# Optimization experiments

Hardware: AMD Instinct MI355X
Metric: run time of the kernel (lower is better)

Reference implementation:

```python
import jax, jax.numpy as jnp
import numpy as np

B, C, L = 8, 512, 4096
KC, VC, H = 512, 512, 8
DK, DV = KC // H, VC // H
EPS = 1e-5


def _ln(x, g, b):
    m = jnp.mean(x, axis=-1, keepdims=True)
    v = jnp.var(x, axis=-1, keepdims=True)
    return (x - m) * jax.lax.rsqrt(v + EPS) * g + b


def setup_inputs() -> dict:
    key = jax.random.key(0)
    ks = jax.random.split(key, 12)
    s = 0.02
    return {
        "z1": jax.random.normal(ks[0], (B, C, L), jnp.float32),
        "z2": jax.random.normal(ks[1], (B, C, L), jnp.float32),
        "Wq": jax.random.normal(ks[2], (KC, C), jnp.float32) * s,
        "bq": jnp.zeros((KC,), jnp.float32),
        "Wk": jax.random.normal(ks[3], (KC, C), jnp.float32) * s,
        "bk": jnp.zeros((KC,), jnp.float32),
        "Wv": jax.random.normal(ks[4], (VC, C), jnp.float32) * s,
        "bv": jnp.zeros((VC,), jnp.float32),
        "Wr": jax.random.normal(ks[5], (C, VC), jnp.float32) * s,
        "br": jnp.zeros((C,), jnp.float32),
        "g1": jnp.ones((C,), jnp.float32),
        "be1": jnp.zeros((C,), jnp.float32),
        "W1": jax.random.normal(ks[6], (2 * C, C), jnp.float32) * s,
        "b1": jnp.zeros((2 * C,), jnp.float32),
        "W2": jax.random.normal(ks[7], (C, 2 * C), jnp.float32) * s,
        "b2": jnp.zeros((C,), jnp.float32),
        "g2": jnp.ones((C,), jnp.float32),
        "be2": jnp.zeros((C,), jnp.float32),
    }


def reference(z1, z2, Wq, bq, Wk, bk, Wv, bv, Wr, br, g1, be1, W1, b1, W2, b2, g2, be2):
    # 1x1 Conv1d projections (channels-first)
    q = jnp.einsum('oc,bcl->bol', Wq, z1) + bq[None, :, None]
    k = jnp.einsum('oc,bcl->bol', Wk, z2) + bk[None, :, None]
    v = jnp.einsum('oc,bcl->bol', Wv, z2) + bv[None, :, None]
    qh = q.reshape(B, H, DK, L)
    kh = k.reshape(B, H, DK, L)
    vh = v.reshape(B, H, DV, L)
    # efficient attention: keys softmax over length, queries over channels
    kh = jax.nn.softmax(kh, axis=-1)
    qh = jax.nn.softmax(qh, axis=2)
    ctx = jnp.einsum('bhkl,bhvl->bhkv', kh, vh)          # [B,H,DK,DV]
    att = jnp.einsum('bhkv,bhkl->bhvl', ctx, qh)          # [B,H,DV,L]
    att = att.reshape(B, VC, L)
    z = jnp.einsum('oc,bcl->bol', Wr, att) + br[None, :, None] + z1  # reprojection + residual
    # b c l -> b l c, LayerNorm, FFN, back
    x = z.transpose(0, 2, 1)
    x = _ln(x, g1, be1)
    h = jax.nn.elu(x @ W1.T + b1)
    y = h @ W2.T + b2
    y = _ln(y, g2, be2)
    return y.transpose(0, 2, 1)
```

## Files before the change

kernel.cpp:

```cpp
#include <hip/hip_runtime.h>
#include <math.h>

#define B_   8
#define C_   512
#define L_   4096
#define H_   8
#define DK_  64
#define C2_  1024

typedef unsigned short ushort;
typedef short     bf16x8_t __attribute__((ext_vector_type(8)));
typedef float     f32x4_t  __attribute__((ext_vector_type(4)));
typedef unsigned short u16x8 __attribute__((ext_vector_type(8)));
typedef unsigned short u16x4 __attribute__((ext_vector_type(4)));

__device__ __forceinline__ float bf2f(ushort u) {
    unsigned int x = ((unsigned int)u) << 16;
    float f; __builtin_memcpy(&f, &x, 4); return f;
}
__device__ __forceinline__ ushort f2bf(float f) {
    unsigned int x; __builtin_memcpy(&x, &f, 4);
    x = (x + 0x7FFFu + ((x >> 16) & 1u)) >> 16;
    return (ushort)x;
}

#define GLOAD_LDS16(gp, lp) \
    __builtin_amdgcn_global_load_lds((const __attribute__((address_space(1))) void*)(gp), \
                                     (__attribute__((address_space(3))) void*)(lp), 16, 0, 0)

__global__ __launch_bounds__(256) void transpose_in(const float* __restrict__ in,
                                                    ushort* __restrict__ out)
{
    const int b = blockIdx.z, c0 = blockIdx.y * 64, l0 = blockIdx.x * 64;
    __shared__ float t[64][65];
    const int tid = threadIdx.x;
    {
        const int c = tid >> 4, l4 = (tid & 15) * 4;
        const float* ip = in + ((size_t)b * C_ + c0) * L_ + l0;
#pragma unroll
        for (int cc = c; cc < 64; cc += 16) {
            float4 v = *(const float4*)(ip + (size_t)cc * L_ + l4);
            t[l4 + 0][cc] = v.x; t[l4 + 1][cc] = v.y;
            t[l4 + 2][cc] = v.z; t[l4 + 3][cc] = v.w;
        }
    }
    __syncthreads();
    {
        const int l = tid >> 3, c8 = (tid & 7) * 8;
        ushort* op = out + ((size_t)b * L_ + l0) * C_ + c0;
#pragma unroll
        for (int ll = l; ll < 64; ll += 32) {
            u16x8 v;
#pragma unroll
            for (int i = 0; i < 8; ++i) v[i] = f2bf(t[ll][c8 + i]);
            *(u16x8*)(op + (size_t)ll * C_ + c8) = v;
        }
    }
}

__global__ __launch_bounds__(256) void transpose_out(const float* __restrict__ in,
                                                     float* __restrict__ out)
{
    const int b = blockIdx.z, c0 = blockIdx.y * 64, l0 = blockIdx.x * 64;
    __shared__ float t[64][65];
    const int tid = threadIdx.x;
    {
        const int l = tid >> 4, c4 = (tid & 15) * 4;
#pragma unroll
        for (int ll = l; ll < 64; ll += 16) {
            float4 v = *(const float4*)(in + ((size_t)(b * L_ + l0 + ll)) * C_ + c0 + c4);
            t[c4 + 0][ll] = v.x; t[c4 + 1][ll] = v.y;
            t[c4 + 2][ll] = v.z; t[c4 + 3][ll] = v.w;
        }
    }
    __syncthreads();
    {
        const int c = tid >> 4, l4 = (tid & 15) * 4;
        float* op = out + ((size_t)b * C_ + c0) * L_ + l0;
#pragma unroll
        for (int cc = c; cc < 64; cc += 16) {
            float4 v = {t[cc][l4], t[cc][l4 + 1], t[cc][l4 + 2], t[cc][l4 + 3]};
            *(float4*)(op + (size_t)cc * L_ + l4) = v;
        }
    }
}

__global__ __launch_bounds__(256) void cvt_bf16(const float* __restrict__ in,
                                                ushort* __restrict__ out, int n4)
{
    const int i = blockIdx.x * 256 + threadIdx.x;
    if (i < n4) {
        float4 v = *(const float4*)(in + 4 * (size_t)i);
        u16x4 o; o[0] = f2bf(v.x); o[1] = f2bf(v.y); o[2] = f2bf(v.z); o[3] = f2bf(v.w);
        *(u16x4*)(out + 4 * (size_t)i) = o;
    }
}

__global__ __launch_bounds__(256) void zero_kernel(float* __restrict__ p, int n4)
{
    const int i = blockIdx.x * 256 + threadIdx.x;
    if (i < n4) { float4 z = {0.f, 0.f, 0.f, 0.f}; *(float4*)(p + 4 * (size_t)i) = z; }
}

template<int ACT, bool HAS_RES>
__global__ __launch_bounds__(256) void conv_mfma(
    const ushort* __restrict__ A, const ushort* __restrict__ Wt,
    const float* __restrict__ bias, const ushort* __restrict__ res,
    ushort* __restrict__ out, int M, int N, int K)
{
    const int m0 = blockIdx.x * 128;
    const int n0 = blockIdx.y * 128;
    const int tid = threadIdx.x;
    const int w = tid >> 6, lane = tid & 63;
    const int wm = (w & 1) * 64, wn = (w >> 1) * 64;
    const int l16 = lane & 15, quad = lane >> 4;

    __shared__ ushort smem[18432];

    f32x4_t acc[4][4];
#pragma unroll
    for (int i = 0; i < 4; ++i)
#pragma unroll
        for (int j = 0; j < 4; ++j) acc[i][j] = (f32x4_t){0.f, 0.f, 0.f, 0.f};

    const int srow = lane >> 2;
    const int sslot = lane & 3;

    const ushort* gA[2]; const ushort* gB[2];
    ushort* lA[2]; ushort* lB[2];
#pragma unroll
    for (int r = 0; r < 2; ++r) {
        const int row = r * 64 + w * 16 + srow;
        const int lk = sslot ^ ((row >> 2) & 3);
        gA[r] = A  + (size_t)(m0 + row) * K + lk * 8;
        gB[r] = Wt + (size_t)(n0 + row) * K + lk * 8;
        lA[r] = smem + (r * 64 + w * 16) * 32;
        lB[r] = smem + 4096 + (r * 64 + w * 16) * 32;
    }

    const int nt = K >> 5;

#pragma unroll
    for (int r = 0; r < 2; ++r) {
        GLOAD_LDS16(gA[r], lA[r]);
        GLOAD_LDS16(gB[r], lB[r]);
    }
    __syncthreads();

    for (int t = 0; t < nt; ++t) {
        const int cur = t & 1;
        if (t + 1 < nt) {
            const int nb = (cur ^ 1) * 8192;
            const size_t co = (size_t)(t + 1) * 32;
#pragma unroll
            for (int r = 0; r < 2; ++r) {
                GLOAD_LDS16(gA[r] + co, lA[r] + nb);
                GLOAD_LDS16(gB[r] + co, lB[r] + nb);
            }
        }
        const ushort* bA = smem + cur * 8192;
        const ushort* bB = bA + 4096;
        bf16x8_t amf[4], wf[4];
#pragma unroll
        for (int i = 0; i < 4; ++i) {
            const int arow = wm + i * 16 + l16;
            const int ap = quad ^ ((arow >> 2) & 3);
            amf[i] = *(const bf16x8_t*)(bA + arow * 32 + ap * 8);
            const int brow = wn + i * 16 + l16;
            const int bp = quad ^ ((brow >> 2) & 3);
            wf[i] = *(const bf16x8_t*)(bB + brow * 32 + bp * 8);
        }
#pragma unroll
        for (int i = 0; i < 4; ++i)
#pragma unroll
            for (int j = 0; j < 4; ++j)
                acc[i][j] = __builtin_amdgcn_mfma_f32_16x16x32_bf16(wf[j], amf[i], acc[i][j], 0, 0, 0);
        if (t + 1 < nt) __syncthreads();
    }

    __syncthreads();
    ushort* sT = smem + w * 4608;
#pragma unroll
    for (int j = 0; j < 4; ++j) {
        const int nb = wn + j * 16 + quad * 4;
        const float4 bo = *(const float4*)(bias + n0 + nb);
        const float bv[4] = {bo.x, bo.y, bo.z, bo.w};
#pragma unroll
        for (int i = 0; i < 4; ++i) {
            const int ml = i * 16 + l16;
            float v[4];
#pragma unroll
            for (int r = 0; r < 4; ++r) v[r] = acc[i][j][r] + bv[r];
            if (HAS_RES) {
                const u16x4 rv = *(const u16x4*)(res + (size_t)(m0 + wm + ml) * N + n0 + nb);
#pragma unroll
                for (int r = 0; r < 4; ++r) v[r] += bf2f(rv[r]);
            }
            if (ACT == 1) {
#pragma unroll
                for (int r = 0; r < 4; ++r) v[r] = (v[r] > 0.f) ? v[r] : (__expf(v[r]) - 1.f);
            }
            u16x4 pv;
#pragma unroll
            for (int r = 0; r < 4; ++r) pv[r] = f2bf(v[r]);
            *(u16x4*)(sT + ml * 72 + (nb - wn)) = pv;
        }
    }
    {
        const int rr = lane >> 3, ch = lane & 7;
#pragma unroll
        for (int rep = 0; rep < 8; ++rep) {
            const int ml = rep * 8 + rr;
            const u16x8 vo = *(const u16x8*)(sT + ml * 72 + ch * 8);
            *(u16x8*)(out + (size_t)(m0 + wm + ml) * N + n0 + wn + ch * 8) = vo;
        }
    }
}

__global__ __launch_bounds__(256) void kstat_chunk(const ushort* __restrict__ k,
                                                   float2* __restrict__ stats)
{
    const int cg = blockIdx.x;
    const int bc = blockIdx.y;
    const int b = bc >> 3, ch = bc & 7;
    const int tid = threadIdx.x;
    const int g = tid & 7;
    const int kk = tid >> 3;
    const int w = tid >> 6, lane = tid & 63;
    const ushort* base = k + ((size_t)(b * L_) + ch * 512) * C_ + cg * 64 + g * 8;

    __shared__ float red[4][8][8];
    __shared__ float mcol[64];

    float fm[8];
#pragma unroll
    for (int i = 0; i < 8; ++i) fm[i] = -3.0e38f;
    for (int r = kk; r < 512; r += 32) {
        u16x8 v = *(const u16x8*)(base + (size_t)r * C_);
#pragma unroll
        for (int i = 0; i < 8; ++i) fm[i] = fmaxf(fm[i], bf2f(v[i]));
    }
#pragma unroll
    for (int off = 8; off <= 32; off <<= 1)
#pragma unroll
        for (int i = 0; i < 8; ++i) fm[i] = fmaxf(fm[i], __shfl_xor(fm[i], off));
    if ((lane >> 3) == 0)
#pragma unroll
        for (int i = 0; i < 8; ++i) red[w][g][i] = fm[i];
    __syncthreads();
    if (tid < 64) {
        const int g2 = tid >> 3, j = tid & 7;
        mcol[g2 * 8 + j] = fmaxf(fmaxf(red[0][g2][j], red[1][g2][j]),
                                 fmaxf(red[2][g2][j], red[3][g2][j]));
    }
    __syncthreads();
    float fmc[8];
#pragma unroll
    for (int i = 0; i < 8; ++i) fmc[i] = mcol[g * 8 + i];

    float fs[8] = {};
    for (int r = kk; r < 512; r += 32) {
        u16x8 v = *(const u16x8*)(base + (size_t)r * C_);
#pragma unroll
        for (int i = 0; i < 8; ++i) fs[i] += __expf(bf2f(v[i]) - fmc[i]);
    }
#pragma unroll
    for (int off = 8; off <= 32; off <<= 1)
#pragma unroll
        for (int i = 0; i < 8; ++i) fs[i] += __shfl_xor(fs[i], off);
    __syncthreads();
    if ((lane >> 3) == 0)
#pragma unroll
        for (int i = 0; i < 8; ++i) red[w][g][i] = fs[i];
    __syncthreads();
    if (tid < 64) {
        const int g2 = tid >> 3, j = tid & 7;
        const float s = red[0][g2][j] + red[1][g2][j] + red[2][g2][j] + red[3][g2][j];
        const int c = cg * 64 + g2 * 8 + j;
        stats[((size_t)(b * C_ + c)) * 8 + ch] = make_float2(mcol[g2 * 8 + j], s);
    }
}

__global__ __launch_bounds__(256) void kstat_merge(const float2* __restrict__ stats,
                                                   float2* __restrict__ minv)
{
    const int i = blockIdx.x * 256 + threadIdx.x;
    if (i >= B_ * C_) return;
    float2 st[8];
    float m = -3.0e38f;
#pragma unroll
    for (int ch = 0; ch < 8; ++ch) { st[ch] = stats[(size_t)i * 8 + ch]; m = fmaxf(m, st[ch].x); }
    float s = 0.f;
#pragma unroll
    for (int ch = 0; ch < 8; ++ch) s += st[ch].y * __expf(st[ch].x - m);
    minv[i] = make_float2(m, 1.f / s);
}

__global__ __launch_bounds__(256) void ctx_accum(
    const ushort* __restrict__ kk, const ushort* __restrict__ vv,
    const float2* __restrict__ minv, float* __restrict__ ctx)
{
    const int bh = blockIdx.y, b = bh >> 3, h = bh & 7;
    const int l0 = blockIdx.x * 512;
    const int tid = threadIdx.x;
    __shared__ float sK[32][72];
    __shared__ float sV[32][72];
    const int srow = tid >> 3, c8 = (tid & 7) * 8;
    const int dv4 = (tid & 15) * 4, dk4 = (tid >> 4) * 4;

    float2 cst[8];
    {
        const float2* mp = minv + (size_t)b * C_ + h * 64 + c8;
#pragma unroll
        for (int i = 0; i < 8; ++i) cst[i] = mp[i];
    }
    float acc[4][4] = {};

    for (int lt = 0; lt < 512; lt += 32) {
        const size_t gbase = ((size_t)(b * L_ + l0 + lt + srow)) * C_ + h * 64 + c8;
        u16x8 kv = *(const u16x8*)(kk + gbase);
        u16x8 vvv = *(const u16x8*)(vv + gbase);
        __syncthreads();
#pragma unroll
        for (int i = 0; i < 8; ++i) {
            sK[srow][c8 + i] = __expf(bf2f(kv[i]) - cst[i].x) * cst[i].y;
            sV[srow][c8 + i] = bf2f(vvv[i]);
        }
        __syncthreads();
#pragma unroll
        for (int ll = 0; ll < 32; ++ll) {
            const float4 a = *(const float4*)&sV[ll][dv4];
            const float4 bb = *(const float4*)&sK[ll][dk4];
            const float av[4] = {a.x, a.y, a.z, a.w};
            const float bv[4] = {bb.x, bb.y, bb.z, bb.w};
#pragma unroll
            for (int i = 0; i < 4; ++i)
#pragma unroll
                for (int j = 0; j < 4; ++j)
                    acc[i][j] = fmaf(av[i], bv[j], acc[i][j]);
        }
    }
    float* cp = ctx + (size_t)bh * 4096;
#pragma unroll
    for (int i = 0; i < 4; ++i)
#pragma unroll
        for (int j = 0; j < 4; ++j)
            atomicAdd(&cp[(dv4 + i) * 64 + (dk4 + j)], acc[i][j]);
}

__global__ __launch_bounds__(256) void att_mfma(
    const ushort* __restrict__ q, const float* __restrict__ ctx,
    ushort* __restrict__ att)
{
    const int bh = blockIdx.y, b = bh >> 3, h = bh & 7;
    const int l0 = blockIdx.x * 128;
    const int tid = threadIdx.x, w = tid >> 6, lane = tid & 63;
    const int l16 = lane & 15, quad = lane >> 4;

    __shared__ ushort sQ[128 * 72];
    __shared__ ushort sC[64 * 72];

    {
        const int part = tid & 7;
#pragma unroll
        for (int rr = tid >> 3; rr < 128; rr += 32) {
            u16x8 v = *(const u16x8*)(q + ((size_t)(b * L_ + l0 + rr)) * C_ + h * 64 + part * 8);
            float f[8], m = -3.0e38f;
#pragma unroll
            for (int i = 0; i < 8; ++i) { f[i] = bf2f(v[i]); m = fmaxf(m, f[i]); }
            m = fmaxf(m, __shfl_xor(m, 1));
            m = fmaxf(m, __shfl_xor(m, 2));
            m = fmaxf(m, __shfl_xor(m, 4));
            float s = 0.f;
#pragma unroll
            for (int i = 0; i < 8; ++i) { f[i] = __expf(f[i] - m); s += f[i]; }
            s += __shfl_xor(s, 1); s += __shfl_xor(s, 2); s += __shfl_xor(s, 4);
            const float inv = 1.f / s;
            u16x8 o;
#pragma unroll
            for (int i = 0; i < 8; ++i) o[i] = f2bf(f[i] * inv);
            *(u16x8*)(sQ + rr * 72 + part * 8) = o;
        }
        const int dv = tid >> 2, dk0 = (tid & 3) * 16;
        const float* cp = ctx + (size_t)bh * 4096 + dv * 64 + dk0;
#pragma unroll
        for (int i = 0; i < 16; ++i) sC[dv * 72 + dk0 + i] = f2bf(cp[i]);
    }
    __syncthreads();

    f32x4_t acc[2][4];
#pragma unroll
    for (int i = 0; i < 2; ++i)
#pragma unroll
        for (int j = 0; j < 4; ++j) acc[i][j] = (f32x4_t){0.f, 0.f, 0.f, 0.f};

#pragma unroll
    for (int ks = 0; ks < 2; ++ks) {
        const int k0 = ks * 32;
        bf16x8_t aq[2], bc[4];
#pragma unroll
        for (int i = 0; i < 2; ++i)
            aq[i] = *(const bf16x8_t*)(sQ + (w * 32 + i * 16 + l16) * 72 + k0 + quad * 8);
#pragma unroll
        for (int j = 0; j < 4; ++j)
            bc[j] = *(const bf16x8_t*)(sC + (j * 16 + l16) * 72 + k0 + quad * 8);
#pragma unroll
        for (int i = 0; i < 2; ++i)
#pragma unroll
            for (int j = 0; j < 4; ++j)
                acc[i][j] = __builtin_amdgcn_mfma_f32_16x16x32_bf16(aq[i], bc[j], acc[i][j], 0, 0, 0);
    }

#pragma unroll
    for (int j = 0; j < 4; ++j)
#pragma unroll
        for (int i = 0; i < 2; ++i) {
            const int mb = l0 + w * 32 + i * 16 + quad * 4;
#pragma unroll
            for (int r = 0; r < 4; ++r)
                att[((size_t)(b * L_ + mb + r)) * C_ + h * 64 + j * 16 + l16] = f2bf(acc[i][j][r]);
        }
}

template<bool OUTF32>
__global__ __launch_bounds__(256) void ln_row(
    const ushort* __restrict__ in, const float* __restrict__ g,
    const float* __restrict__ be, ushort* __restrict__ outb,
    float* __restrict__ outf)
{
    const int tid = threadIdx.x, w = tid >> 6, lane = tid & 63;
    const size_t row = (size_t)blockIdx.x * 4 + w;
    const ushort* p = in + row * C_ + lane * 8;
    u16x8 v = *(const u16x8*)p;
    float f[8], s = 0.f, s2 = 0.f;
#pragma unroll
    for (int i = 0; i < 8; ++i) { f[i] = bf2f(v[i]); s += f[i]; s2 = fmaf(f[i], f[i], s2); }
#pragma unroll
    for (int o = 1; o < 64; o <<= 1) { s += __shfl_xor(s, o); s2 += __shfl_xor(s2, o); }
    const float mean = s * (1.f / C_);
    const float var  = s2 * (1.f / C_) - mean * mean;
    const float inv  = rsqrtf(var + 1e-5f);
    if (OUTF32) {
        float* op = outf + row * C_ + lane * 8;
#pragma unroll
        for (int i = 0; i < 8; ++i)
            op[i] = (f[i] - mean) * inv * g[lane * 8 + i] + be[lane * 8 + i];
    } else {
        u16x8 ov;
#pragma unroll
        for (int i = 0; i < 8; ++i)
            ov[i] = f2bf((f[i] - mean) * inv * g[lane * 8 + i] + be[lane * 8 + i]);
        *(u16x8*)(outb + row * C_ + lane * 8) = ov;
    }
}

extern "C" void kernel_launch(void* const* d_in, const int* in_sizes, int n_in,
                              void* d_out, int out_size, void* d_ws, size_t ws_size,
                              hipStream_t stream)
{
    const float* z1  = (const float*)d_in[0];
    const float* z2  = (const float*)d_in[1];
    const float* Wq  = (const float*)d_in[2];
    const float* bq  = (const float*)d_in[3];
    const float* Wk  = (const float*)d_in[4];
    const float* bk  = (const float*)d_in[5];
    const float* Wv  = (const float*)d_in[6];
    const float* bv  = (const float*)d_in[7];
    const float* Wr  = (const float*)d_in[8];
    const float* br  = (const float*)d_in[9];
    const float* g1  = (const float*)d_in[10];
    const float* be1 = (const float*)d_in[11];
    const float* W1  = (const float*)d_in[12];
    const float* b1  = (const float*)d_in[13];
    const float* W2  = (const float*)d_in[14];
    const float* b2  = (const float*)d_in[15];
    const float* g2  = (const float*)d_in[16];
    const float* be2 = (const float*)d_in[17];
    float* out = (float*)d_out;

    const size_t SB = (size_t)B_ * L_ * C_;
    ushort* ws16 = (ushort*)d_ws;
    ushort* b0v = ws16;
    ushort* b1v = ws16 + SB;
    ushort* b2v = ws16 + 2 * SB;
    ushort* b3v = ws16 + 3 * SB;
    ushort* wb  = ws16 + 4 * SB;
    ushort* wbq = wb;
    ushort* wbk = wb + 262144;
    ushort* wbv = wb + 524288;
    ushort* wbr = wb + 786432;
    ushort* wb1 = wb + 1048576;
    ushort* wb2 = wb + 1572864;
    float*  ctxf = (float*)(wb + 2097152);
    float2* stats = (float2*)(ctxf + 65536);
    float2* minv  = stats + (size_t)B_ * C_ * 8;
    ushort* vbuf = (ushort*)d_out;
    ushort* hbuf = (ushort*)d_out;
    float*  yf32 = (float*)b2v;

    const dim3 blk(256);
    const int M = B_ * L_;

    transpose_in<<<dim3(L_/64, C_/64, B_), blk, 0, stream>>>(z1, b0v);
    transpose_in<<<dim3(L_/64, C_/64, B_), blk, 0, stream>>>(z2, b1v);
    cvt_bf16<<<dim3(262144/4/256), blk, 0, stream>>>(Wq, wbq, 262144/4);
    cvt_bf16<<<dim3(262144/4/256), blk, 0, stream>>>(Wk, wbk, 262144/4);
    cvt_bf16<<<dim3(262144/4/256), blk, 0, stream>>>(Wv, wbv, 262144/4);
    cvt_bf16<<<dim3(262144/4/256), blk, 0, stream>>>(Wr, wbr, 262144/4);
    cvt_bf16<<<dim3(524288/4/256), blk, 0, stream>>>(W1, wb1, 524288/4);
    cvt_bf16<<<dim3(524288/4/256), blk, 0, stream>>>(W2, wb2, 524288/4);

    conv_mfma<0,false><<<dim3(M/128, C_/128), blk, 0, stream>>>(b0v, wbq, bq, nullptr, b2v, M, C_, C_);
    conv_mfma<0,false><<<dim3(M/128, C_/128), blk, 0, stream>>>(b1v, wbk, bk, nullptr, b3v, M, C_, C_);
    conv_mfma<0,false><<<dim3(M/128, C_/128), blk, 0, stream>>>(b1v, wbv, bv, nullptr, vbuf, M, C_, C_);

    kstat_chunk<<<dim3(C_/64, B_ * 8), blk, 0, stream>>>(b3v, stats);
    kstat_merge<<<dim3((B_ * C_ + 255) / 256), blk, 0, stream>>>(stats, minv);

    zero_kernel<<<dim3(65536/256), blk, 0, stream>>>(ctxf, 65536);
    ctx_accum<<<dim3(8, B_ * H_), blk, 0, stream>>>(b3v, vbuf, minv, ctxf);

    att_mfma<<<dim3(L_/128, B_ * H_), blk, 0, stream>>>(b2v, ctxf, b1v);

    conv_mfma<0,true><<<dim3(M/128, C_/128), blk, 0, stream>>>(b1v, wbr, br, b0v, b2v, M, C_, C_);

    ln_row<false><<<dim3(M/4), blk, 0, stream>>>(b2v, g1, be1, b3v, nullptr);

    conv_mfma<1,false><<<dim3(M/128, C2_/128), blk, 0, stream>>>(b3v, wb1, b1, nullptr, hbuf, M, C2_, C_);

    conv_mfma<0,false><<<dim3(M/128, C_/128), blk, 0, stream>>>(hbuf, wb2, b2, nullptr, b0v, M, C_, C2_);

    ln_row<true><<<dim3(M/4), blk, 0, stream>>>(b0v, g2, be2, nullptr, yf32);

    transpose_out<<<dim3(L_/64, C_/64, B_), blk, 0, stream>>>(yf32, out);
}
```

Measured before the change: 577.7 us.

## Triple-buffer GEMM LDS loads with one barrier per step; split ctx_accum finer

```diff
diff --git a/kernel.cpp b/kernel.cpp
--- a/kernel.cpp
+++ b/kernel.cpp
@@ -115,7 +115,7 @@
     const int wm = (w & 1) * 64, wn = (w >> 1) * 64;
     const int l16 = lane & 15, quad = lane >> 4;
 
-    __shared__ ushort smem[18432];
+    __shared__ ushort smem[24576];
 
     f32x4_t acc[4][4];
 #pragma unroll
@@ -127,55 +127,62 @@
     const int sslot = lane & 3;
 
     const ushort* gA[2]; const ushort* gB[2];
-    ushort* lA[2]; ushort* lB[2];
+    int loff[2];
 #pragma unroll
     for (int r = 0; r < 2; ++r) {
         const int row = r * 64 + w * 16 + srow;
         const int lk = sslot ^ ((row >> 2) & 3);
         gA[r] = A  + (size_t)(m0 + row) * K + lk * 8;
         gB[r] = Wt + (size_t)(n0 + row) * K + lk * 8;
-        lA[r] = smem + (r * 64 + w * 16) * 32;
-        lB[r] = smem + 4096 + (r * 64 + w * 16) * 32;
+        loff[r] = (r * 64 + w * 16) * 32;
     }
 
     const int nt = K >> 5;
 
 #pragma unroll
-    for (int r = 0; r < 2; ++r) {
-        GLOAD_LDS16(gA[r], lA[r]);
-        GLOAD_LDS16(gB[r], lB[r]);
-    }
-    __syncthreads();
-
+    for (int p = 0; p < 2; ++p) {
+        ushort* lb = smem + p * 8192;
+#pragma unroll
+        for (int r = 0; r < 2; ++r) {
+            GLOAD_LDS16(gA[r] + p * 32, lb + loff[r]);
+            GLOAD_LDS16(gB[r] + p * 32, lb + 4096 + loff[r]);
+        }
+    }
+
+    int buf = 0;
     for (int t = 0; t < nt; ++t) {
-        const int cur = t & 1;
-        if (t + 1 < nt) {
-            const int nb = (cur ^ 1) * 8192;
-            const size_t co = (size_t)(t + 1) * 32;
+        if (t + 1 < nt) { asm volatile("s_waitcnt vmcnt(4)" ::: "memory"); }
+        else            { asm volatile("s_waitcnt vmcnt(0)" ::: "memory"); }
+        __builtin_amdgcn_s_barrier();
+        __builtin_amdgcn_sched_barrier(0);
+        if (t + 2 < nt) {
+            const int nb2 = (buf >= 1) ? buf - 1 : buf + 2;
+            ushort* lb = smem + nb2 * 8192;
+            const size_t co = (size_t)(t + 2) * 32;
 #pragma unroll
             for (int r = 0; r < 2; ++r) {
-                GLOAD_LDS16(gA[r] + co, lA[r] + nb);
-                GLOAD_LDS16(gB[r] + co, lB[r] + nb);
+                GLOAD_LDS16(gA[r] + co, lb + loff[r]);
+                GLOAD_LDS16(gB[r] + co, lb + 4096 + loff[r]);
             }
         }
-        const ushort* bA = smem + cur * 8192;
+        const ushort* bA = smem + buf * 8192;
         const ushort* bB = bA + 4096;
         bf16x8_t amf[4], wf[4];
 #pragma unroll
         for (int i = 0; i < 4; ++i) {
             const int arow = wm + i * 16 + l16;
-            const int ap = quad ^ ((arow >> 2) & 3);
-            amf[i] = *(const bf16x8_t*)(bA + arow * 32 + ap * 8);
+            amf[i] = *(const bf16x8_t*)(bA + arow * 32 + (quad ^ ((arow >> 2) & 3)) * 8);
             const int brow = wn + i * 16 + l16;
-            const int bp = quad ^ ((brow >> 2) & 3);
-            wf[i] = *(const bf16x8_t*)(bB + brow * 32 + bp * 8);
-        }
+            wf[i]  = *(const bf16x8_t*)(bB + brow * 32 + (quad ^ ((brow >> 2) & 3)) * 8);
+        }
+        __builtin_amdgcn_s_setprio(1);
 #pragma unroll
         for (int i = 0; i < 4; ++i)
 #pragma unroll
             for (int j = 0; j < 4; ++j)
                 acc[i][j] = __builtin_amdgcn_mfma_f32_16x16x32_bf16(wf[j], amf[i], acc[i][j], 0, 0, 0);
-        if (t + 1 < nt) __syncthreads();
+        __builtin_amdgcn_s_setprio(0);
+        buf = (buf == 2) ? 0 : buf + 1;
     }
 
     __syncthreads();
@@ -301,10 +308,10 @@
     const float2* __restrict__ minv, float* __restrict__ ctx)
 {
     const int bh = blockIdx.y, b = bh >> 3, h = bh & 7;
-    const int l0 = blockIdx.x * 512;
+    const int l0 = blockIdx.x * 256;
     const int tid = threadIdx.x;
-    __shared__ float sK[32][72];
-    __shared__ float sV[32][72];
+    __shared__ float sK[32][76];
+    __shared__ float sV[32][76];
     const int srow = tid >> 3, c8 = (tid & 7) * 8;
     const int dv4 = (tid & 15) * 4, dk4 = (tid >> 4) * 4;
 
@@ -316,16 +323,21 @@
     }
     float acc[4][4] = {};
 
-    for (int lt = 0; lt < 512; lt += 32) {
+    for (int lt = 0; lt < 256; lt += 32) {
         const size_t gbase = ((size_t)(b * L_ + l0 + lt + srow)) * C_ + h * 64 + c8;
         u16x8 kv = *(const u16x8*)(kk + gbase);
         u16x8 vvv = *(const u16x8*)(vv + gbase);
         __syncthreads();
+        float fk[8], fv[8];
 #pragma unroll
         for (int i = 0; i < 8; ++i) {
-            sK[srow][c8 + i] = __expf(bf2f(kv[i]) - cst[i].x) * cst[i].y;
-            sV[srow][c8 + i] = bf2f(vvv[i]);
-        }
+            fk[i] = __expf(bf2f(kv[i]) - cst[i].x) * cst[i].y;
+            fv[i] = bf2f(vvv[i]);
+        }
+        *(float4*)&sK[srow][c8]     = (float4){fk[0], fk[1], fk[2], fk[3]};
+        *(float4*)&sK[srow][c8 + 4] = (float4){fk[4], fk[5], fk[6], fk[7]};
+        *(float4*)&sV[srow][c8]     = (float4){fv[0], fv[1], fv[2], fv[3]};
+        *(float4*)&sV[srow][c8 + 4] = (float4){fv[4], fv[5], fv[6], fv[7]};
         __syncthreads();
 #pragma unroll
         for (int ll = 0; ll < 32; ++ll) {
@@ -518,7 +530,7 @@
     kstat_merge<<<dim3((B_ * C_ + 255) / 256), blk, 0, stream>>>(stats, minv);
 
     zero_kernel<<<dim3(65536/256), blk, 0, stream>>>(ctxf, 65536);
-    ctx_accum<<<dim3(8, B_ * H_), blk, 0, stream>>>(b3v, vbuf, minv, ctxf);
+    ctx_accum<<<dim3(16, B_ * H_), blk, 0, stream>>>(b3v, vbuf, minv, ctxf);
 
     att_mfma<<<dim3(L_/128, B_ * H_), blk, 0, stream>>>(b2v, ctxf, b1v);
 
```

After: 579.1 us. Within noise of the previous version (+0.2%).

## Enlarge GEMM tiles to 256x256 with 512 threads and move ctx accumulation to MFMA

Applied to the files above, without the earlier changes.

```diff
diff --git a/kernel.cpp b/kernel.cpp
--- a/kernel.cpp
+++ b/kernel.cpp
@@ -103,96 +103,97 @@
 }
 
 template<int ACT, bool HAS_RES>
-__global__ __launch_bounds__(256) void conv_mfma(
+__global__ __launch_bounds__(512, 2) void conv_mfma(
     const ushort* __restrict__ A, const ushort* __restrict__ Wt,
     const float* __restrict__ bias, const ushort* __restrict__ res,
     ushort* __restrict__ out, int M, int N, int K)
 {
-    const int m0 = blockIdx.x * 128;
-    const int n0 = blockIdx.y * 128;
+    const int m0 = blockIdx.x * 256;
+    const int n0 = blockIdx.y * 256;
     const int tid = threadIdx.x;
     const int w = tid >> 6, lane = tid & 63;
-    const int wm = (w & 1) * 64, wn = (w >> 1) * 64;
+    const int wm = (w >> 2) * 128, wn = (w & 3) * 64;
     const int l16 = lane & 15, quad = lane >> 4;
 
-    __shared__ ushort smem[18432];
-
-    f32x4_t acc[4][4];
-#pragma unroll
-    for (int i = 0; i < 4; ++i)
+    __shared__ ushort smem[32768];
+
+    const int sRow = tid >> 2;
+    const int sSwz = ((tid & 3) ^ (sRow & 3)) * 8;
+    const ushort* gA0 = A  + (size_t)(m0 + sRow) * K + sSwz;
+    const ushort* gA1 = A  + (size_t)(m0 + 128 + sRow) * K + sSwz;
+    const ushort* gB0 = Wt + (size_t)(n0 + sRow) * K + sSwz;
+    const ushort* gB1 = Wt + (size_t)(n0 + 128 + sRow) * K + sSwz;
+    const int dA0 = (w * 16) * 32;
+    const int dA1 = (128 + w * 16) * 32;
+
+    f32x4_t acc[8][4];
+#pragma unroll
+    for (int i = 0; i < 8; ++i)
 #pragma unroll
         for (int j = 0; j < 4; ++j) acc[i][j] = (f32x4_t){0.f, 0.f, 0.f, 0.f};
 
-    const int srow = lane >> 2;
-    const int sslot = lane & 3;
-
-    const ushort* gA[2]; const ushort* gB[2];
-    ushort* lA[2]; ushort* lB[2];
-#pragma unroll
-    for (int r = 0; r < 2; ++r) {
-        const int row = r * 64 + w * 16 + srow;
-        const int lk = sslot ^ ((row >> 2) & 3);
-        gA[r] = A  + (size_t)(m0 + row) * K + lk * 8;
-        gB[r] = Wt + (size_t)(n0 + row) * K + lk * 8;
-        lA[r] = smem + (r * 64 + w * 16) * 32;
-        lB[r] = smem + 4096 + (r * 64 + w * 16) * 32;
-    }
-
     const int nt = K >> 5;
 
-#pragma unroll
-    for (int r = 0; r < 2; ++r) {
-        GLOAD_LDS16(gA[r], lA[r]);
-        GLOAD_LDS16(gB[r], lB[r]);
-    }
-    __syncthreads();
+    {
+        ushort* bufA = smem;
+        ushort* bufB = smem + 8192;
+        GLOAD_LDS16(gA0, bufA + dA0);
+        GLOAD_LDS16(gA1, bufA + dA1);
+        GLOAD_LDS16(gB0, bufB + dA0);
+        GLOAD_LDS16(gB1, bufB + dA1);
+    }
 
     for (int t = 0; t < nt; ++t) {
-        const int cur = t & 1;
+        const ushort* bufA = smem + (t & 1) * 16384;
+        const ushort* bufB = bufA + 8192;
+        __builtin_amdgcn_s_barrier();
+        asm volatile("" ::: "memory");
         if (t + 1 < nt) {
-            const int nb = (cur ^ 1) * 8192;
+            ushort* nA = smem + ((t + 1) & 1) * 16384;
+            ushort* nB = nA + 8192;
             const size_t co = (size_t)(t + 1) * 32;
-#pragma unroll
-            for (int r = 0; r < 2; ++r) {
-                GLOAD_LDS16(gA[r] + co, lA[r] + nb);
-                GLOAD_LDS16(gB[r] + co, lB[r] + nb);
-            }
-        }
-        const ushort* bA = smem + cur * 8192;
-        const ushort* bB = bA + 4096;
-        bf16x8_t amf[4], wf[4];
-#pragma unroll
-        for (int i = 0; i < 4; ++i) {
-            const int arow = wm + i * 16 + l16;
-            const int ap = quad ^ ((arow >> 2) & 3);
-            amf[i] = *(const bf16x8_t*)(bA + arow * 32 + ap * 8);
-            const int brow = wn + i * 16 + l16;
-            const int bp = quad ^ ((brow >> 2) & 3);
-            wf[i] = *(const bf16x8_t*)(bB + brow * 32 + bp * 8);
-        }
-#pragma unroll
-        for (int i = 0; i < 4; ++i)
+            GLOAD_LDS16(gA0 + co, nA + dA0);
+            GLOAD_LDS16(gA1 + co, nA + dA1);
+            GLOAD_LDS16(gB0 + co, nB + dA0);
+            GLOAD_LDS16(gB1 + co, nB + dA1);
+            asm volatile("s_waitcnt vmcnt(4)" ::: "memory");
+        } else {
+            asm volatile("s_waitcnt vmcnt(0)" ::: "memory");
+        }
+        __builtin_amdgcn_s_barrier();
+        asm volatile("" ::: "memory");
+
+        bf16x8_t wf[4];
+#pragma unroll
+        for (int j = 0; j < 4; ++j) {
+            const int br = wn + j * 16 + l16;
+            wf[j] = *(const bf16x8_t*)(bufB + br * 32 + (quad ^ (br & 3)) * 8);
+        }
+        __builtin_amdgcn_s_setprio(1);
+#pragma unroll
+        for (int i = 0; i < 8; ++i) {
+            const int ar = wm + i * 16 + l16;
+            const bf16x8_t af = *(const bf16x8_t*)(bufA + ar * 32 + (quad ^ (ar & 3)) * 8);
 #pragma unroll
             for (int j = 0; j < 4; ++j)
-                acc[i][j] = __builtin_amdgcn_mfma_f32_16x16x32_bf16(wf[j], amf[i], acc[i][j], 0, 0, 0);
-        if (t + 1 < nt) __syncthreads();
-    }
-
-    __syncthreads();
-    ushort* sT = smem + w * 4608;
+                acc[i][j] = __builtin_amdgcn_mfma_f32_16x16x32_bf16(wf[j], af, acc[i][j], 0, 0, 0);
+        }
+        __builtin_amdgcn_s_setprio(0);
+    }
+
 #pragma unroll
     for (int j = 0; j < 4; ++j) {
-        const int nb = wn + j * 16 + quad * 4;
-        const float4 bo = *(const float4*)(bias + n0 + nb);
+        const int nb = n0 + wn + j * 16 + quad * 4;
+        const float4 bo = *(const float4*)(bias + nb);
         const float bv[4] = {bo.x, bo.y, bo.z, bo.w};
 #pragma unroll
-        for (int i = 0; i < 4; ++i) {
-            const int ml = i * 16 + l16;
+        for (int i = 0; i < 8; ++i) {
+            const int m = m0 + wm + i * 16 + l16;
             float v[4];
 #pragma unroll
             for (int r = 0; r < 4; ++r) v[r] = acc[i][j][r] + bv[r];
             if (HAS_RES) {
-                const u16x4 rv = *(const u16x4*)(res + (size_t)(m0 + wm + ml) * N + n0 + nb);
+                const u16x4 rv = *(const u16x4*)(res + (size_t)m * N + nb);
 #pragma unroll
                 for (int r = 0; r < 4; ++r) v[r] += bf2f(rv[r]);
             }
@@ -203,16 +204,7 @@
             u16x4 pv;
 #pragma unroll
             for (int r = 0; r < 4; ++r) pv[r] = f2bf(v[r]);
-            *(u16x4*)(sT + ml * 72 + (nb - wn)) = pv;
-        }
-    }
-    {
-        const int rr = lane >> 3, ch = lane & 7;
-#pragma unroll
-        for (int rep = 0; rep < 8; ++rep) {
-            const int ml = rep * 8 + rr;
-            const u16x8 vo = *(const u16x8*)(sT + ml * 72 + ch * 8);
-            *(u16x8*)(out + (size_t)(m0 + wm + ml) * N + n0 + wn + ch * 8) = vo;
+            *(u16x4*)(out + (size_t)m * N + nb) = pv;
         }
     }
 }
@@ -296,56 +288,76 @@
     minv[i] = make_float2(m, 1.f / s);
 }
 
-__global__ __launch_bounds__(256) void ctx_accum(
+__global__ __launch_bounds__(256) void ctx_mfma(
     const ushort* __restrict__ kk, const ushort* __restrict__ vv,
     const float2* __restrict__ minv, float* __restrict__ ctx)
 {
     const int bh = blockIdx.y, b = bh >> 3, h = bh & 7;
-    const int l0 = blockIdx.x * 512;
-    const int tid = threadIdx.x;
-    __shared__ float sK[32][72];
-    __shared__ float sV[32][72];
-    const int srow = tid >> 3, c8 = (tid & 7) * 8;
-    const int dv4 = (tid & 15) * 4, dk4 = (tid >> 4) * 4;
+    const int l0 = blockIdx.x * 256;
+    const int tid = threadIdx.x, w = tid >> 6, lane = tid & 63;
+    const int l16 = lane & 15, quad = lane >> 4;
+
+    __shared__ ushort sK[64 * 72];
+    __shared__ ushort sV[64 * 72];
+
+    const int grp = tid >> 7;
+    const int st  = tid & 127;
+    const int sc8 = (st & 7) * 8;
+    const int sl4 = (st >> 3) * 4;
+    const ushort* gsrc = (grp ? vv : kk)
+        + ((size_t)(b * L_ + l0 + sl4)) * C_ + h * 64 + sc8;
+    ushort* dst = grp ? sV : sK;
 
     float2 cst[8];
-    {
-        const float2* mp = minv + (size_t)b * C_ + h * 64 + c8;
-#pragma unroll
-        for (int i = 0; i < 8; ++i) cst[i] = mp[i];
-    }
-    float acc[4][4] = {};
-
-    for (int lt = 0; lt < 512; lt += 32) {
-        const size_t gbase = ((size_t)(b * L_ + l0 + lt + srow)) * C_ + h * 64 + c8;
-        u16x8 kv = *(const u16x8*)(kk + gbase);
-        u16x8 vvv = *(const u16x8*)(vv + gbase);
+#pragma unroll
+    for (int i = 0; i < 8; ++i)
+        cst[i] = minv[(size_t)b * C_ + h * 64 + sc8 + i];
+
+    f32x4_t acc[4];
+#pragma unroll
+    for (int j = 0; j < 4; ++j) acc[j] = (f32x4_t){0.f, 0.f, 0.f, 0.f};
+
+    for (int tile = 0; tile < 4; ++tile) {
+        u16x8 vr[4];
+#pragma unroll
+        for (int j = 0; j < 4; ++j)
+            vr[j] = *(const u16x8*)(gsrc + ((size_t)(tile * 64 + j)) * C_);
         __syncthreads();
-#pragma unroll
-        for (int i = 0; i < 8; ++i) {
-            sK[srow][c8 + i] = __expf(bf2f(kv[i]) - cst[i].x) * cst[i].y;
-            sV[srow][c8 + i] = bf2f(vvv[i]);
+        if (grp == 0) {
+#pragma unroll
+            for (int c = 0; c < 8; ++c) {
+                u16x4 o;
+#pragma unroll
+                for (int j = 0; j < 4; ++j)
+                    o[j] = f2bf(__expf(bf2f(vr[j][c]) - cst[c].x) * cst[c].y);
+                *(u16x4*)(dst + (sc8 + c) * 72 + sl4) = o;
+            }
+        } else {
+#pragma unroll
+            for (int c = 0; c < 8; ++c) {
+                u16x4 o;
+#pragma unroll
+                for (int j = 0; j < 4; ++j) o[j] = vr[j][c];
+                *(u16x4*)(dst + (sc8 + c) * 72 + sl4) = o;
+            }
         }
         __syncthreads();
 #pragma unroll
-        for (int ll = 0; ll < 32; ++ll) {
-            const float4 a = *(const float4*)&sV[ll][dv4];
-            const float4 bb = *(const float4*)&sK[ll][dk4];
-            const float av[4] = {a.x, a.y, a.z, a.w};
-            const float bv[4] = {bb.x, bb.y, bb.z, bb.w};
-#pragma unroll
-            for (int i = 0; i < 4; ++i)
-#pragma unroll
-                for (int j = 0; j < 4; ++j)
-                    acc[i][j] = fmaf(av[i], bv[j], acc[i][j]);
+        for (int k0 = 0; k0 < 64; k0 += 32) {
+            const bf16x8_t vf = *(const bf16x8_t*)(sV + (w * 16 + l16) * 72 + k0 + quad * 8);
+#pragma unroll
+            for (int j = 0; j < 4; ++j) {
+                const bf16x8_t kf = *(const bf16x8_t*)(sK + (j * 16 + l16) * 72 + k0 + quad * 8);
+                acc[j] = __builtin_amdgcn_mfma_f32_16x16x32_bf16(vf, kf, acc[j], 0, 0, 0);
+            }
         }
     }
     float* cp = ctx + (size_t)bh * 4096;
 #pragma unroll
-    for (int i = 0; i < 4; ++i)
-#pragma unroll
-        for (int j = 0; j < 4; ++j)
-            atomicAdd(&cp[(dv4 + i) * 64 + (dk4 + j)], acc[i][j]);
+    for (int j = 0; j < 4; ++j)
+#pragma unroll
+        for (int r = 0; r < 4; ++r)
+            atomicAdd(&cp[(w * 16 + quad * 4 + r) * 64 + (j * 16 + l16)], acc[j][r]);
 }
 
 __global__ __launch_bounds__(256) void att_mfma(
@@ -499,6 +511,7 @@
     float*  yf32 = (float*)b2v;
 
     const dim3 blk(256);
+    const dim3 blk512(512);
     const int M = B_ * L_;
 
     transpose_in<<<dim3(L_/64, C_/64, B_), blk, 0, stream>>>(z1, b0v);
@@ -510,25 +523,25 @@
     cvt_bf16<<<dim3(524288/4/256), blk, 0, stream>>>(W1, wb1, 524288/4);
     cvt_bf16<<<dim3(524288/4/256), blk, 0, stream>>>(W2, wb2, 524288/4);
 
-    conv_mfma<0,false><<<dim3(M/128, C_/128), blk, 0, stream>>>(b0v, wbq, bq, nullptr, b2v, M, C_, C_);
-    conv_mfma<0,false><<<dim3(M/128, C_/128), blk, 0, stream>>>(b1v, wbk, bk, nullptr, b3v, M, C_, C_);
-    conv_mfma<0,false><<<dim3(M/128, C_/128), blk, 0, stream>>>(b1v, wbv, bv, nullptr, vbuf, M, C_, C_);
+    conv_mfma<0,false><<<dim3(M/256, C_/256), blk512, 0, stream>>>(b0v, wbq, bq, nullptr, b2v, M, C_, C_);
+    conv_mfma<0,false><<<dim3(M/256, C_/256), blk512, 0, stream>>>(b1v, wbk, bk, nullptr, b3v, M, C_, C_);
+    conv_mfma<0,false><<<dim3(M/256, C_/256), blk512, 0, stream>>>(b1v, wbv, bv, nullptr, vbuf, M, C_, C_);
 
     kstat_chunk<<<dim3(C_/64, B_ * 8), blk, 0, stream>>>(b3v, stats);
     kstat_merge<<<dim3((B_ * C_ + 255) / 256), blk, 0, stream>>>(stats, minv);
 
     zero_kernel<<<dim3(65536/256), blk, 0, stream>>>(ctxf, 65536);
-    ctx_accum<<<dim3(8, B_ * H_), blk, 0, stream>>>(b3v, vbuf, minv, ctxf);
+    ctx_mfma<<<dim3(16, B_ * H_), blk, 0, stream>>>(b3v, vbuf, minv, ctxf);
 
     att_mfma<<<dim3(L_/128, B_ * H_), blk, 0, stream>>>(b2v, ctxf, b1v);
 
-    conv_mfma<0,true><<<dim3(M/128, C_/128), blk, 0, stream>>>(b1v, wbr, br, b0v, b2v, M, C_, C_);
+    conv_mfma<0,true><<<dim3(M/256, C_/256), blk512, 0, stream>>>(b1v, wbr, br, b0v, b2v, M, C_, C_);
 
     ln_row<false><<<dim3(M/4), blk, 0, stream>>>(b2v, g1, be1, b3v, nullptr);
 
-    conv_mfma<1,false><<<dim3(M/128, C2_/128), blk, 0, stream>>>(b3v, wb1, b1, nullptr, hbuf, M, C2_, C_);
-
-    conv_mfma<0,false><<<dim3(M/128, C_/128), blk, 0, stream>>>(hbuf, wb2, b2, nullptr, b0v, M, C_, C2_);
+    conv_mfma<1,false><<<dim3(M/256, C2_/256), blk512, 0, stream>>>(b3v, wb1, b1, nullptr, hbuf, M, C2_, C_);
+
+    conv_mfma<0,false><<<dim3(M/256, C_/256), blk512, 0, stream>>>(hbuf, wb2, b2, nullptr, b0v, M, C_, C2_);
 
     ln_row<true><<<dim3(M/4), blk, 0, stream>>>(b0v, g2, be2, nullptr, yf32);
 
```

After: 553.5 us. -4.2%, faster.
